# Performance work log

Measured on AMD Instinct MI355X. Metric: run time of the kernel, lower is better.

Reference implementation:

```python
import jax, jax.numpy as jnp
import numpy as np

HID = 200
HALF = 100  # TreeLSTM hidden = hidden_size // 2
N_EDUS = 32768
N_STEPS = 2 * N_EDUS - 1


def setup_inputs() -> dict:
    key = jax.random.key(0)
    ks = jax.random.split(key, 16)
    s = 0.05  # keep logits / gates in a sane range
    d = {}
    d["enc_cls"] = jax.random.normal(ks[0], (N_EDUS, 768), jnp.float32)
    d["W_proj"] = jax.random.normal(ks[1], (HID, 768), jnp.float32) * s
    d["b_proj"] = jax.random.normal(ks[2], (HID,), jnp.float32) * s
    d["missing_node"] = jax.random.uniform(ks[3], (HID,), jnp.float32)
    d["W_act"] = jax.random.normal(ks[4], (2, 3 * HID), jnp.float32) * s
    d["b_act"] = jax.random.normal(ks[5], (2,), jnp.float32) * s
    d["W_lab"] = jax.random.normal(ks[6], (19, 3 * HID), jnp.float32) * s
    d["b_lab"] = jax.random.normal(ks[7], (19,), jnp.float32) * s
    d["W_dir"] = jax.random.normal(ks[8], (3, 3 * HID), jnp.float32) * s
    d["b_dir"] = jax.random.normal(ks[9], (3,), jnp.float32) * s
    d["W_tree"] = jax.random.normal(ks[10], (5 * HALF, 2 * HALF), jnp.float32) * s
    d["b_tree"] = jax.random.normal(ks[11], (5 * HALF,), jnp.float32) * s
    d["gold_action"] = jax.random.randint(ks[12], (N_STEPS,), 0, 2, jnp.int32)
    d["gold_label"] = jax.random.randint(ks[13], (N_STEPS,), 0, 19, jnp.int32)
    d["gold_direction"] = jax.random.randint(ks[14], (N_STEPS,), 0, 3, jnp.int32)
    return d


def reference(enc_cls, W_proj, b_proj, missing_node, W_act, b_act,
              W_lab, b_lab, W_dir, b_dir, W_tree, b_tree,
              gold_action, gold_label, gold_direction):
    N = enc_cls.shape[0]
    S = 2 * N - 1
    # BERT CLS -> project (dropout is identity in eval)
    enc = enc_cls @ W_proj.T + b_proj  # [N, 200]

    # deterministic left-branching gold schedule: shift, then (shift, reduce)*
    t = jnp.arange(S)
    is_shift = (t == 0) | (t % 2 == 1)

    def treelstm(e1, e2):
        # embeddings are concat(h, c), each HALF
        h1, c1 = e1[:HALF], e1[HALF:]
        h2, c2 = e2[:HALF], e2[HALF:]
        g = W_tree @ jnp.concatenate([h1, h2]) + b_tree  # [5*HALF]
        i, f1, f2, o, u = jnp.split(g, 5)
        c = jax.nn.sigmoid(i) * jnp.tanh(u) \
            + jax.nn.sigmoid(f1) * c1 + jax.nn.sigmoid(f2) * c2
        h = jax.nn.sigmoid(o) * jnp.tanh(c)
        return jnp.concatenate([h, c])

    def ce(logits, y):
        # CrossEntropyLoss for a single example
        return jax.nn.logsumexp(logits) - logits[y]

    def step(carry, xs):
        s1, s0, ptr = carry
        shift, ga, gl, gd = xs
        b = jnp.where(ptr < N, enc[jnp.minimum(ptr, N - 1)], missing_node)
        feats = jnp.concatenate([s1, s0, b])  # [600]
        loss = (ce(W_act @ feats + b_act, ga)
                + ce(W_lab @ feats + b_lab, gl)
                + ce(W_dir @ feats + b_dir, gd))
        merged = treelstm(s1, s0)
        s0n = jnp.where(shift, b, merged)
        s1n = jnp.where(shift, s0, missing_node)
        ptrn = ptr + shift.astype(ptr.dtype)
        return (s1n, s0n, ptrn), loss

    init = (missing_node, missing_node, jnp.int32(0))
    (_, root, _), losses = jax.lax.scan(
        step, init, (is_shift, gold_action, gold_label, gold_direction))
    return losses.sum()
```

## Files before the change

kernel.cpp:

```cpp
#include <hip/hip_runtime.h>
#include <cstdint>

#define HID 200
#define HALF 100
#define N_EDUS 32768
#define N_STEPS (2*N_EDUS - 1)
#define KMAX 32766
#define PSTRIDE 500

typedef __fp16 h2v __attribute__((ext_vector_type(2)));

__global__ __launch_bounds__(256) void gemm_bt(const float* __restrict__ A, int lda,
    const float* __restrict__ B, int ldb, const float* __restrict__ bias,
    float* __restrict__ C, int ldc, int M, int N, int K)
{
    __shared__ float As[32][68];
    __shared__ float Bs[32][68];
    const int tid = threadIdx.x;
    const int tx = tid & 15, ty = tid >> 4;
    const int m0 = blockIdx.x * 64, n0 = blockIdx.y * 64;
    float acc[4][4] = {};
    for (int kc = 0; kc < K; kc += 32) {
        const int kk = tid & 31, r0 = tid >> 5;
        #pragma unroll
        for (int p = 0; p < 8; ++p) {
            const int mm = r0 + p * 8;
            const int m = m0 + mm, n = n0 + mm, kg = kc + kk;
            As[kk][mm] = (m < M && kg < K) ? A[(size_t)m * lda + kg] : 0.f;
            Bs[kk][mm] = (n < N && kg < K) ? B[(size_t)n * ldb + kg] : 0.f;
        }
        __syncthreads();
        #pragma unroll
        for (int kk2 = 0; kk2 < 32; ++kk2) {
            const float4 a = *(const float4*)&As[kk2][tx * 4];
            const float4 b = *(const float4*)&Bs[kk2][ty * 4];
            const float av[4] = {a.x, a.y, a.z, a.w};
            const float bv[4] = {b.x, b.y, b.z, b.w};
            #pragma unroll
            for (int r = 0; r < 4; ++r)
                #pragma unroll
                for (int c = 0; c < 4; ++c)
                    acc[r][c] += av[r] * bv[c];
        }
        __syncthreads();
    }
    #pragma unroll
    for (int r = 0; r < 4; ++r) {
        const int m = m0 + tx * 4 + r;
        if (m >= M) continue;
        #pragma unroll
        for (int c = 0; c < 4; ++c) {
            const int n = n0 + ty * 4 + c;
            if (n < N) C[(size_t)m * ldc + n] = acc[r][c] + (bias ? bias[n] : 0.f);
        }
    }
}

__global__ void prep_kernel(const float* __restrict__ W_act, const float* __restrict__ W_lab,
    const float* __restrict__ W_dir, const float* __restrict__ miss,
    float* __restrict__ WAB, float* __restrict__ WBC,
    float* __restrict__ msAB, float* __restrict__ msBC, float* __restrict__ out)
{
    const int tid = threadIdx.x;
    if (tid == 0) out[0] = 0.f;
    for (int i = tid; i < 48 * 200; i += 256) {
        const int r = i / 200, c = i % 200;
        const int rr = r % 24;
        const float* src = (rr < 2) ? (W_act + rr * 600)
                         : (rr < 21) ? (W_lab + (rr - 2) * 600)
                                     : (W_dir + (rr - 21) * 600);
        WAB[i] = src[c + (r < 24 ? 0 : 200)];
        WBC[i] = src[c + (r < 24 ? 200 : 400)];
    }
    __syncthreads();
    if (tid < 48) {
        float sA = 0.f, sB = 0.f;
        for (int c = 0; c < 200; ++c) {
            sA += WAB[tid * 200 + c] * miss[c];
            sB += WBC[tid * 200 + c] * miss[c];
        }
        msAB[tid] = sA;
        msBC[tid] = sB;
    }
}

__global__ __launch_bounds__(256) void pack_w16(const float* __restrict__ W_tree,
                                                unsigned int* __restrict__ W16)
{
    const int i = blockIdx.x * 256 + threadIdx.x;
    if (i >= 5 * 4 * 13 * 128) return;
    const int d = i & 127, r = i >> 7;
    const int t = r % 13, gq = r / 13, q = gq & 3, g = gq >> 2;
    const int pst[4] = {0, 13, 26, 38}, pct[4] = {13, 13, 12, 12};
    unsigned int val = 0;
    if (t < pct[q] && d < 100) {
        const int p = pst[q] + t;
        const float w0 = W_tree[(size_t)(g * 100 + d) * 200 + 2 * p];
        const float w1 = W_tree[(size_t)(g * 100 + d) * 200 + 2 * p + 1];
        h2v h = __builtin_amdgcn_cvt_pkrtz(w0, w1);
        __builtin_memcpy(&val, &h, 4);
    }
    W16[i] = val;
}

__device__ __forceinline__ float sigf(float x) {
    return __builtin_amdgcn_rcpf(1.f + __expf(-x));
}
__device__ __forceinline__ float tanhf_(float x) {
    return 1.f - 2.f * __builtin_amdgcn_rcpf(1.f + __expf(2.f * x));
}
__device__ __forceinline__ h2v u2h(unsigned int u) { h2v h; __builtin_memcpy(&h, &u, 4); return h; }

#define BAR() asm volatile("s_waitcnt lgkmcnt(0)\n\ts_barrier" ::: "memory")
#define KEEP(x) asm volatile("" : "+v"(x))
#define DPPADD(x, c) ((x) + __int_as_float(__builtin_amdgcn_update_dpp(0, __float_as_int(x), (c), 0xF, 0xF, true)))

#define BODY(U, DOLOAD) \
{ \
    const unsigned int* hb = (const unsigned int*)(&hbufh[(U) & 1][0]) + pstq; \
    float ac0 = 0.f, ac1 = 0.f, ac2 = 0.f, ac3 = 0.f, ac4 = 0.f; \
    _Pragma("unroll") \
    for (int t = 0; t < 13; ++t) { \
        const h2v hwt = u2h(hb[t]); \
        ac0 = __builtin_amdgcn_fdot2(u2h(W[0][t]), hwt, ac0, false); \
        ac1 = __builtin_amdgcn_fdot2(u2h(W[1][t]), hwt, ac1, false); \
        ac2 = __builtin_amdgcn_fdot2(u2h(W[2][t]), hwt, ac2, false); \
        ac3 = __builtin_amdgcn_fdot2(u2h(W[3][t]), hwt, ac3, false); \
        ac4 = __builtin_amdgcn_fdot2(u2h(W[4][t]), hwt, ac4, false); \
    } \
    ac0 = DPPADD(ac0, 0xB1); ac0 = DPPADD(ac0, 0x4E); \
    ac1 = DPPADD(ac1, 0xB1); ac1 = DPPADD(ac1, 0x4E); \
    ac2 = DPPADD(ac2, 0xB1); ac2 = DPPADD(ac2, 0x4E); \
    ac3 = DPPADD(ac3, 0xB1); ac3 = DPPADD(ac3, 0x4E); \
    ac4 = DPPADD(ac4, 0xB1); ac4 = DPPADD(ac4, 0x4E); \
    const float prim = (q == 0) ? ac0 : (q == 1) ? ac1 : (q == 2) ? ac2 : ac3; \
    const float sg = sigf(prim + pa[U]); \
    const float mult = (q == 0) ? tanhf_(ac4 + px[U]) \
                     : (q == 1) ? c_reg \
                     : (q == 2) ? px[U] : 0.f; \
    if (DOLOAD) { pa[U] = *pPA; pPA += PSTRIDE; px[U] = *pPX; pPX += strX; } \
    float a = sg * mult; \
    a = DPPADD(a, 0xB1); \
    a = DPPADD(a, 0x4E); \
    if (q == 3) { \
        const float h = sg * tanhf_(a); \
        hbufh[((U) & 1) ^ 1][d] = (_Float16)h; \
        if (act) *pMst = h; \
    } else if (q == 1) { \
        c_reg = a; \
        if (act) *pMst = a; \
    } \
    pMst += 200; \
    BAR(); \
}

__attribute__((amdgpu_flat_work_group_size(512, 512), amdgpu_waves_per_eu(2, 2)))
__global__ void chain_kernel(const float* __restrict__ enc,
    const unsigned int* __restrict__ W16, const float* __restrict__ P, float* __restrict__ M)
{
    const int T = threadIdx.x;
    const int d = T >> 2, q = T & 3;
    const bool act = (d < 100);
    __shared__ _Float16 hbufh[2][128];

    if (T < 200) M[T] = enc[T];

    unsigned int W[5][13];
    #pragma unroll
    for (int g = 0; g < 5; ++g)
        #pragma unroll
        for (int t = 0; t < 13; ++t)
            W[g][t] = W16[(size_t)(((g * 4 + q) * 13 + t) * 128) + d];
    #pragma unroll
    for (int g = 0; g < 5; ++g)
        #pragma unroll
        for (int t = 0; t < 13; ++t)
            KEEP(W[g][t]);

    const int pstA[4] = {0, 13, 26, 38};
    const int pstq = pstA[q];
    const int goA = q * 100 + d;

    const float* pA0 = P + goA;
    const float* pX0 = (q == 0) ? (P + 400 + d)
                     : (q == 2) ? (enc + 100 + d) : P;
    const int strX   = (q == 0) ? PSTRIDE : (q == 2) ? 200 : 0;

    float c_reg = 0.f;
    if (act && q == 1) c_reg = enc[100 + d];
    if (q == 0) hbufh[0][d] = (_Float16)enc[d];

    float pa[4], px[4];
    #pragma unroll
    for (int kk = 1; kk <= 4; ++kk) {
        pa[kk - 1] = pA0[(size_t)kk * PSTRIDE];
        px[kk - 1] = pX0[(size_t)kk * strX];
    }
    const float* pPA = pA0 + (size_t)5 * PSTRIDE;
    const float* pPX = pX0 + (size_t)5 * strX;
    float* pMst = M + 200 + ((q == 3) ? d : 100 + d);
    BAR();

    for (int base = 1; base <= KMAX - 9; base += 4) {
        BODY(0, true);
        BODY(1, true);
        BODY(2, true);
        BODY(3, true);
    }
    BODY(0, true);
    BODY(1, true);
    BODY(2, false);
    BODY(3, false);
    BODY(0, false);
    BODY(1, false);
}

__global__ __launch_bounds__(256) void loss_kernel(const float* __restrict__ TM,
    const float* __restrict__ TE, const float* __restrict__ msAB, const float* __restrict__ msBC,
    const float* __restrict__ b_act, const float* __restrict__ b_lab, const float* __restrict__ b_dir,
    const int* __restrict__ ga, const int* __restrict__ gl, const int* __restrict__ gd,
    float* __restrict__ out)
{
    const int t = blockIdx.x * 256 + threadIdx.x;
    float loss = 0.f;
    if (t < N_STEPS) {
        const float *v1, *v0, *vb;
        if (t == 0)      { v1 = msAB; v0 = msAB + 24; vb = TE + 24; }
        else if (t == 1) { v1 = msAB; v0 = TE;        vb = TE + 48 + 24; }
        else if ((t & 1) == 0) {
            const int k = t >> 1;
            v1 = TM + (size_t)(k - 1) * 48;
            v0 = TE + (size_t)k * 48;
            vb = (k < N_EDUS - 1) ? (TE + (size_t)(k + 1) * 48 + 24) : (msBC + 24);
        } else {
            const int k = t >> 1;
            v1 = msAB;
            v0 = TM + (size_t)k * 48 + 24;
            vb = TE + (size_t)(k + 1) * 48 + 24;
        }
        float l[24];
        #pragma unroll
        for (int j = 0; j < 24; ++j) l[j] = v1[j] + v0[j] + vb[j];
        l[0] += b_act[0]; l[1] += b_act[1];
        #pragma unroll
        for (int j = 0; j < 19; ++j) l[2 + j] += b_lab[j];
        #pragma unroll
        for (int j = 0; j < 3; ++j) l[21 + j] += b_dir[j];
        const int ya = ga[t], yl = gl[t], yd = gd[t];
        {
            const float m = fmaxf(l[0], l[1]);
            const float sum = __expf(l[0] - m) + __expf(l[1] - m);
            loss += m + __logf(sum) - (ya == 0 ? l[0] : l[1]);
        }
        {
            float m = l[2];
            #pragma unroll
            for (int j = 1; j < 19; ++j) m = fmaxf(m, l[2 + j]);
            float sum = 0.f, ly = 0.f;
            #pragma unroll
            for (int j = 0; j < 19; ++j) {
                sum += __expf(l[2 + j] - m);
                if (j == yl) ly = l[2 + j];
            }
            loss += m + __logf(sum) - ly;
        }
        {
            const float m = fmaxf(fmaxf(l[21], l[22]), l[23]);
            const float sum = __expf(l[21] - m) + __expf(l[22] - m) + __expf(l[23] - m);
            const float ly = (yd == 0) ? l[21] : (yd == 1 ? l[22] : l[23]);
            loss += m + __logf(sum) - ly;
        }
    }
    #pragma unroll
    for (int off = 32; off > 0; off >>= 1) loss += __shfl_down(loss, off, 64);
    __shared__ float wsum[4];
    const int lane = threadIdx.x & 63, wv = threadIdx.x >> 6;
    if (lane == 0) wsum[wv] = loss;
    __syncthreads();
    if (threadIdx.x == 0) atomicAdd(out, wsum[0] + wsum[1] + wsum[2] + wsum[3]);
}

extern "C" void kernel_launch(void* const* d_in, const int* in_sizes, int n_in,
                              void* d_out, int out_size, void* d_ws, size_t ws_size,
                              hipStream_t stream) {
    const float* enc_cls = (const float*)d_in[0];
    const float* W_proj  = (const float*)d_in[1];
    const float* b_proj  = (const float*)d_in[2];
    const float* miss    = (const float*)d_in[3];
    const float* W_act   = (const float*)d_in[4];
    const float* b_act   = (const float*)d_in[5];
    const float* W_lab   = (const float*)d_in[6];
    const float* b_lab   = (const float*)d_in[7];
    const float* W_dir   = (const float*)d_in[8];
    const float* b_dir   = (const float*)d_in[9];
    const float* W_tree  = (const float*)d_in[10];
    const float* b_tree  = (const float*)d_in[11];
    const int*   ga      = (const int*)d_in[12];
    const int*   gl      = (const int*)d_in[13];
    const int*   gd      = (const int*)d_in[14];
    float* out = (float*)d_out;

    float* ws   = (float*)d_ws;
    float* enc  = ws;
    float* Mar  = ws + 6553600;
    float* P    = ws + 13107000;
    float* WAB  = ws + 29490500;
    float* WBC  = WAB + 9600;
    float* msAB = WBC + 9600;
    float* msBC = msAB + 48;
    unsigned int* W16 = (unsigned int*)(msBC + 48);
    float* TM = P;
    float* TE = P + 1572816;

    gemm_bt<<<dim3(512, 4, 1), 256, 0, stream>>>(enc_cls, 768, W_proj, 768, b_proj,
                                                 enc, 200, N_EDUS, 200, 768);
    gemm_bt<<<dim3(512, 8, 1), 256, 0, stream>>>(enc + 200, 200, W_tree + 100, 200, b_tree,
                                                 P + PSTRIDE, PSTRIDE, KMAX, 500, 100);
    prep_kernel<<<1, 256, 0, stream>>>(W_act, W_lab, W_dir, miss, WAB, WBC, msAB, msBC, out);
    pack_w16<<<130, 256, 0, stream>>>(W_tree, W16);
    chain_kernel<<<1, 512, 0, stream>>>(enc, W16, P, Mar);
    gemm_bt<<<dim3(512, 1, 1), 256, 0, stream>>>(Mar, 200, WAB, 200, nullptr,
                                                 TM, 48, KMAX + 1, 48, 200);
    gemm_bt<<<dim3(512, 1, 1), 256, 0, stream>>>(enc, 200, WBC, 200, nullptr,
                                                 TE, 48, N_EDUS, 48, 200);
    loss_kernel<<<dim3(256, 1, 1), 256, 0, stream>>>(TM, TE, msAB, msBC,
                                                     b_act, b_lab, b_dir, ga, gl, gd, out);
}
```

Before: 20.53 ms.

## Move sequential TreeLSTM chain matvec onto MFMA 16x16x32 f16 instructions

The serial chain kernel's per-step 500x100 matvec is recast as MFMA 16x16x32 f16 operations. Seven waves each own 16 output rows, and their weights are repacked into MFMA A-fragments held in registers. The step's h vector is the B operand, and each lane picks its own row's result from the accumulator, so the DPP cross-lane reductions and the split of gate work across four threads are gone. Each active lane now computes all five gates for its row itself. This is meant to shorten the per-step latency of the critical serial loop, at the cost of a mostly wasted 16-column MFMA (only one useful column) and the fixed latency of a chain of MFMA instructions.

Result: faster. 19.36 ms (-5.7%).

```diff
diff --git a/kernel.cpp b/kernel.cpp
--- a/kernel.cpp
+++ b/kernel.cpp
@@ -9,6 +9,8 @@
 #define PSTRIDE 500
 
 typedef __fp16 h2v __attribute__((ext_vector_type(2)));
+typedef _Float16 f16x8 __attribute__((ext_vector_type(8)));
+typedef float f32x4 __attribute__((ext_vector_type(4)));
 
 __global__ __launch_bounds__(256) void gemm_bt(const float* __restrict__ A, int lda,
     const float* __restrict__ B, int ldb, const float* __restrict__ bias,
@@ -84,23 +86,30 @@
     }
 }
 
-__global__ __launch_bounds__(256) void pack_w16(const float* __restrict__ W_tree,
-                                                unsigned int* __restrict__ W16)
+__global__ __launch_bounds__(256) void pack_wa(const float* __restrict__ W_tree,
+                                               uint4* __restrict__ WA)
 {
     const int i = blockIdx.x * 256 + threadIdx.x;
-    if (i >= 5 * 4 * 13 * 128) return;
-    const int d = i & 127, r = i >> 7;
-    const int t = r % 13, gq = r / 13, q = gq & 3, g = gq >> 2;
-    const int pst[4] = {0, 13, 26, 38}, pct[4] = {13, 13, 12, 12};
-    unsigned int val = 0;
-    if (t < pct[q] && d < 100) {
-        const int p = pst[q] + t;
-        const float w0 = W_tree[(size_t)(g * 100 + d) * 200 + 2 * p];
-        const float w1 = W_tree[(size_t)(g * 100 + d) * 200 + 2 * p + 1];
+    if (i >= 8960) return;
+    const int lane = i & 63, f = i >> 6;
+    const int kc = f & 3, gw = f >> 2;
+    const int w = gw % 7, g = gw / 7;
+    const int row = w * 16 + (lane & 15);
+    const int kb = kc * 32 + (lane >> 4) * 8;
+    unsigned int dws[4];
+    #pragma unroll
+    for (int dw = 0; dw < 4; ++dw) {
+        const int k0 = kb + dw * 2;
+        float w0 = 0.f, w1 = 0.f;
+        if (row < 100) {
+            if (k0 < 100)     w0 = W_tree[(size_t)(g * 100 + row) * 200 + k0];
+            if (k0 + 1 < 100) w1 = W_tree[(size_t)(g * 100 + row) * 200 + k0 + 1];
+        }
         h2v h = __builtin_amdgcn_cvt_pkrtz(w0, w1);
-        __builtin_memcpy(&val, &h, 4);
-    }
-    W16[i] = val;
+        __builtin_memcpy(&dws[dw], &h, 4);
+    }
+    uint4 v; v.x = dws[0]; v.y = dws[1]; v.z = dws[2]; v.w = dws[3];
+    WA[i] = v;
 }
 
 __device__ __forceinline__ float sigf(float x) {
@@ -109,96 +118,92 @@
 __device__ __forceinline__ float tanhf_(float x) {
     return 1.f - 2.f * __builtin_amdgcn_rcpf(1.f + __expf(2.f * x));
 }
-__device__ __forceinline__ h2v u2h(unsigned int u) { h2v h; __builtin_memcpy(&h, &u, 4); return h; }
 
 #define BAR() asm volatile("s_waitcnt lgkmcnt(0)\n\ts_barrier" ::: "memory")
-#define KEEP(x) asm volatile("" : "+v"(x))
-#define DPPADD(x, c) ((x) + __int_as_float(__builtin_amdgcn_update_dpp(0, __float_as_int(x), (c), 0xF, 0xF, true)))
+
+#define SELR(v) ((rsel & 2) ? ((rsel & 1) ? (v)[3] : (v)[2]) : ((rsel & 1) ? (v)[1] : (v)[0]))
 
 #define BODY(U, DOLOAD) \
 { \
-    const unsigned int* hb = (const unsigned int*)(&hbufh[(U) & 1][0]) + pstq; \
-    float ac0 = 0.f, ac1 = 0.f, ac2 = 0.f, ac3 = 0.f, ac4 = 0.f; \
+    const uint4* hb = (const uint4*)(&hbuf[(U) & 1][0]); \
+    f16x8 bb[4]; \
+    { \
+        uint4 t0 = hb[kgrp];      uint4 t1 = hb[4 + kgrp]; \
+        uint4 t2 = hb[8 + kgrp];  uint4 t3 = hb[12 + kgrp]; \
+        __builtin_memcpy(&bb[0], &t0, 16); __builtin_memcpy(&bb[1], &t1, 16); \
+        __builtin_memcpy(&bb[2], &t2, 16); __builtin_memcpy(&bb[3], &t3, 16); \
+    } \
+    f32x4 acc[5]; \
     _Pragma("unroll") \
-    for (int t = 0; t < 13; ++t) { \
-        const h2v hwt = u2h(hb[t]); \
-        ac0 = __builtin_amdgcn_fdot2(u2h(W[0][t]), hwt, ac0, false); \
-        ac1 = __builtin_amdgcn_fdot2(u2h(W[1][t]), hwt, ac1, false); \
-        ac2 = __builtin_amdgcn_fdot2(u2h(W[2][t]), hwt, ac2, false); \
-        ac3 = __builtin_amdgcn_fdot2(u2h(W[3][t]), hwt, ac3, false); \
-        ac4 = __builtin_amdgcn_fdot2(u2h(W[4][t]), hwt, ac4, false); \
+    for (int g = 0; g < 5; ++g) acc[g] = (f32x4){0.f, 0.f, 0.f, 0.f}; \
+    _Pragma("unroll") \
+    for (int kc = 0; kc < 4; ++kc) { \
+        _Pragma("unroll") \
+        for (int g = 0; g < 5; ++g) \
+            acc[g] = __builtin_amdgcn_mfma_f32_16x16x32_f16(A[g][kc], bb[kc], acc[g], 0, 0, 0); \
     } \
-    ac0 = DPPADD(ac0, 0xB1); ac0 = DPPADD(ac0, 0x4E); \
-    ac1 = DPPADD(ac1, 0xB1); ac1 = DPPADD(ac1, 0x4E); \
-    ac2 = DPPADD(ac2, 0xB1); ac2 = DPPADD(ac2, 0x4E); \
-    ac3 = DPPADD(ac3, 0xB1); ac3 = DPPADD(ac3, 0x4E); \
-    ac4 = DPPADD(ac4, 0xB1); ac4 = DPPADD(ac4, 0x4E); \
-    const float prim = (q == 0) ? ac0 : (q == 1) ? ac1 : (q == 2) ? ac2 : ac3; \
-    const float sg = sigf(prim + pa[U]); \
-    const float mult = (q == 0) ? tanhf_(ac4 + px[U]) \
-                     : (q == 1) ? c_reg \
-                     : (q == 2) ? px[U] : 0.f; \
-    if (DOLOAD) { pa[U] = *pPA; pPA += PSTRIDE; px[U] = *pPX; pPX += strX; } \
-    float a = sg * mult; \
-    a = DPPADD(a, 0xB1); \
-    a = DPPADD(a, 0x4E); \
-    if (q == 3) { \
-        const float h = sg * tanhf_(a); \
-        hbufh[((U) & 1) ^ 1][d] = (_Float16)h; \
-        if (act) *pMst = h; \
-    } else if (q == 1) { \
-        c_reg = a; \
-        if (act) *pMst = a; \
+    const float gi  = SELR(acc[0]) + pr[U][0]; \
+    const float gf1 = SELR(acc[1]) + pr[U][1]; \
+    const float gf2 = SELR(acc[2]) + pr[U][2]; \
+    const float go  = SELR(acc[3]) + pr[U][3]; \
+    const float gu  = SELR(acc[4]) + pr[U][4]; \
+    const float c2v = pr[U][5]; \
+    if (DOLOAD) { \
+        pr[U][0] = pP[0];   pr[U][1] = pP[100]; pr[U][2] = pP[200]; \
+        pr[U][3] = pP[300]; pr[U][4] = pP[400]; pP += PSTRIDE; \
+        pr[U][5] = *pE; pE += HID; \
     } \
-    pMst += 200; \
+    const float cnew = sigf(gi) * tanhf_(gu) + sigf(gf1) * c_sel + sigf(gf2) * c2v; \
+    const float hnew = sigf(go) * tanhf_(cnew); \
+    c_sel = cnew; \
+    if (act) { \
+        pM[0] = hnew; pM[100] = cnew; \
+        hbuf[((U) & 1) ^ 1][row_c] = (_Float16)hnew; \
+    } \
+    pM += HID; \
     BAR(); \
 }
 
-__attribute__((amdgpu_flat_work_group_size(512, 512), amdgpu_waves_per_eu(2, 2)))
+__attribute__((amdgpu_flat_work_group_size(448, 448), amdgpu_waves_per_eu(2, 2)))
 __global__ void chain_kernel(const float* __restrict__ enc,
-    const unsigned int* __restrict__ W16, const float* __restrict__ P, float* __restrict__ M)
+    const uint4* __restrict__ WA, const float* __restrict__ P, float* __restrict__ M)
 {
     const int T = threadIdx.x;
-    const int d = T >> 2, q = T & 3;
-    const bool act = (d < 100);
-    __shared__ _Float16 hbufh[2][128];
+    const int wave = T >> 6, lane = T & 63;
+    const int col = lane & 15, kgrp = lane >> 4;
+    const int rsel = col & 3;
+    const int row_c = wave * 16 + kgrp * 4 + rsel;
+    const bool act = (col < 4) && (row_c < 100);
+    __shared__ __align__(16) _Float16 hbuf[2][128];
 
     if (T < 200) M[T] = enc[T];
-
-    unsigned int W[5][13];
+    if (T < 128) {
+        hbuf[0][T] = (T < 100) ? (_Float16)enc[T] : (_Float16)0.f;
+        hbuf[1][T] = (_Float16)0.f;
+    }
+
+    f16x8 A[5][4];
     #pragma unroll
     for (int g = 0; g < 5; ++g)
         #pragma unroll
-        for (int t = 0; t < 13; ++t)
-            W[g][t] = W16[(size_t)(((g * 4 + q) * 13 + t) * 128) + d];
-    #pragma unroll
-    for (int g = 0; g < 5; ++g)
-        #pragma unroll
-        for (int t = 0; t < 13; ++t)
-            KEEP(W[g][t]);
-
-    const int pstA[4] = {0, 13, 26, 38};
-    const int pstq = pstA[q];
-    const int goA = q * 100 + d;
-
-    const float* pA0 = P + goA;
-    const float* pX0 = (q == 0) ? (P + 400 + d)
-                     : (q == 2) ? (enc + 100 + d) : P;
-    const int strX   = (q == 0) ? PSTRIDE : (q == 2) ? 200 : 0;
-
-    float c_reg = 0.f;
-    if (act && q == 1) c_reg = enc[100 + d];
-    if (q == 0) hbufh[0][d] = (_Float16)enc[d];
-
-    float pa[4], px[4];
-    #pragma unroll
-    for (int kk = 1; kk <= 4; ++kk) {
-        pa[kk - 1] = pA0[(size_t)kk * PSTRIDE];
-        px[kk - 1] = pX0[(size_t)kk * strX];
-    }
-    const float* pPA = pA0 + (size_t)5 * PSTRIDE;
-    const float* pPX = pX0 + (size_t)5 * strX;
-    float* pMst = M + 200 + ((q == 3) ? d : 100 + d);
+        for (int kc = 0; kc < 4; ++kc) {
+            uint4 t = WA[((g * 7 + wave) * 4 + kc) * 64 + lane];
+            __builtin_memcpy(&A[g][kc], &t, 16);
+        }
+
+    float c_sel = enc[100 + row_c];
+
+    float pr[4][6];
+    #pragma unroll
+    for (int u = 0; u < 4; ++u) {
+        #pragma unroll
+        for (int g = 0; g < 5; ++g)
+            pr[u][g] = P[(size_t)(1 + u) * PSTRIDE + g * 100 + row_c];
+        pr[u][5] = enc[(size_t)(1 + u) * HID + 100 + row_c];
+    }
+    const float* pP = P + (size_t)5 * PSTRIDE + row_c;
+    const float* pE = enc + (size_t)5 * HID + 100 + row_c;
+    float* pM = M + HID + row_c;
     BAR();
 
     for (int base = 1; base <= KMAX - 9; base += 4) {
@@ -308,7 +313,7 @@
     float* WBC  = WAB + 9600;
     float* msAB = WBC + 9600;
     float* msBC = msAB + 48;
-    unsigned int* W16 = (unsigned int*)(msBC + 48);
+    uint4* WA   = (uint4*)(msBC + 48);
     float* TM = P;
     float* TE = P + 1572816;
 
@@ -317,8 +322,8 @@
     gemm_bt<<<dim3(512, 8, 1), 256, 0, stream>>>(enc + 200, 200, W_tree + 100, 200, b_tree,
                                                  P + PSTRIDE, PSTRIDE, KMAX, 500, 100);
     prep_kernel<<<1, 256, 0, stream>>>(W_act, W_lab, W_dir, miss, WAB, WBC, msAB, msBC, out);
-    pack_w16<<<130, 256, 0, stream>>>(W_tree, W16);
-    chain_kernel<<<1, 512, 0, stream>>>(enc, W16, P, Mar);
+    pack_wa<<<35, 256, 0, stream>>>(W_tree, WA);
+    chain_kernel<<<1, 448, 0, stream>>>(enc, WA, P, Mar);
     gemm_bt<<<dim3(512, 1, 1), 256, 0, stream>>>(Mar, 200, WAB, 200, nullptr,
                                                  TM, 48, KMAX + 1, 48, 200);
     gemm_bt<<<dim3(512, 1, 1), 256, 0, stream>>>(enc, 200, WBC, 200, nullptr,
```
